# Performance work log

Hardware: AMD Instinct MI355X
Metric: run time of the kernel (lower is better)

## Reference

```python
import jax, jax.numpy as jnp
import numpy as np

BN_EPS = 1e-5


def binary_activation(x):
    # ReActNet binary activation: forward = sign(x), backward = d/dx of
    # piecewise polynomial approximation (straight-through estimator).
    out_fwd = jnp.sign(x)
    out3 = jnp.where(x < -1.0, -1.0,
           jnp.where(x < 0.0, x * x + 2.0 * x,
           jnp.where(x < 1.0, -x * x + 2.0 * x, 1.0)))
    return jax.lax.stop_gradient(out_fwd - out3) + out3


def binarize_weights(w):
    # HardBinaryConv: per-output-channel scale = mean(|w|) (detached),
    # binary weight = scale * sign(w), STE through clamp(w, -1, 1).
    scale = jax.lax.stop_gradient(jnp.mean(jnp.abs(w), axis=(1, 2, 3), keepdims=True))
    bw_no_grad = scale * jnp.sign(w)
    cw = jnp.clip(w, -1.0, 1.0)
    return jax.lax.stop_gradient(bw_no_grad - cw) + cw


def setup_inputs() -> dict:
    key = jax.random.key(0)
    k1, k2, k3, k4 = jax.random.split(key, 4)
    x = jax.random.normal(k1, (32, 256, 56, 56), dtype=jnp.float32)
    weight = jax.random.normal(k2, (256, 256, 3, 3), dtype=jnp.float32) * 0.05  # OIHW
    gamma = 1.0 + 0.1 * jax.random.normal(k3, (256,), dtype=jnp.float32)
    beta = 0.1 * jax.random.normal(k4, (256,), dtype=jnp.float32)
    return {"x": x, "weight": weight, "gamma": gamma, "beta": beta}


def reference(x, weight, gamma, beta):
    xa = binary_activation(x)                       # [B, Cin, H, W], values in {-1, 0, +1}
    bw = binarize_weights(weight)                   # [Cout, Cin, 3, 3]
    y = jax.lax.conv_general_dilated(
        xa, bw,
        window_strides=(1, 1),
        padding=((1, 1), (1, 1)),
        dimension_numbers=("NCHW", "OIHW", "NCHW"))  # [B, Cout, H, W]
    # BatchNorm2d, training-mode batch statistics over (N, H, W)
    mean = jnp.mean(y, axis=(0, 2, 3), keepdims=True)
    var = jnp.var(y, axis=(0, 2, 3), keepdims=True)
    yn = (y - mean) * jax.lax.rsqrt(var + BN_EPS)
    y = yn * gamma[None, :, None, None] + beta[None, :, None, None]
    return jax.nn.relu(y)
```

## Files before the change

### kernel.cpp

```cpp
#include <hip/hip_runtime.h>
#include <stdint.h>
#include <type_traits>

#define CIN   256
#define COUT  256
#define HH    56
#define WW    56
#define HW    3136
#define BATCH 32
#define NPIX  (BATCH*HW)
#define PH    58
#define PW    58
#define PPIX  (PH*PW)
#define KTOT  2304
#define BKB   128
#define NKIT  (KTOT/BKB)

#define NBIN  (HW/64*BATCH)
#define NBRD  (BATCH*PH)

typedef int8_t  i8;
typedef int     intx4  __attribute__((ext_vector_type(4)));
typedef short   short8 __attribute__((ext_vector_type(8)));
typedef float   floatx4 __attribute__((ext_vector_type(4)));

__device__ __forceinline__ void gload_lds16(const i8* g, void* lds_base) {
    __builtin_amdgcn_global_load_lds(
        (const __attribute__((address_space(1))) void*)g,
        (__attribute__((address_space(3))) void*)lds_base,
        16, 0, 0);
}

__global__ __launch_bounds__(256) void front(const float* __restrict__ x,
                                             const float* __restrict__ w,
                                             i8* __restrict__ xs,
                                             i8* __restrict__ wg,
                                             float* __restrict__ scale,
                                             float* __restrict__ bnsum,
                                             float* __restrict__ bnsumsq) {
    int b = blockIdx.x;
    int t = threadIdx.x;
    if (b < NBIN) {
        __shared__ int lds[64 * 65];
        int p0 = (b % 49) * 64;
        int n  = b / 49;
        const float* xin = x + (size_t)n * CIN * HW;
        int pq  = t & 15;
        int cqg = t >> 4;
#pragma unroll
        for (int q = 0; q < 4; ++q) {
            int cbase = q * 64 + cqg * 4;
            floatx4 f[4];
#pragma unroll
            for (int r = 0; r < 4; ++r)
                f[r] = __builtin_nontemporal_load(
                    (const floatx4*)&xin[(size_t)(cbase + r) * HW + p0 + pq * 4]);
#pragma unroll
            for (int j = 0; j < 4; ++j) {
                int packed = 0;
#pragma unroll
                for (int r = 0; r < 4; ++r) {
                    float v = f[r][j];
                    int s = (v > 0.f) ? 1 : ((v < 0.f) ? -1 : 0);
                    packed |= (s & 0xff) << (8 * r);
                }
                lds[(pq * 4 + j) * 65 + q * 16 + cqg] = packed;
            }
        }
        __syncthreads();
        int ci = t & 15;
#pragma unroll
        for (int q = 0; q < 4; ++q) {
            int pi = (t >> 4) + q * 16;
            int4 v;
            v.x = lds[pi * 65 + ci * 4 + 0];
            v.y = lds[pi * 65 + ci * 4 + 1];
            v.z = lds[pi * 65 + ci * 4 + 2];
            v.w = lds[pi * 65 + ci * 4 + 3];
            int p = p0 + pi;
            int h = p / WW, ww = p - (p / WW) * WW;
            *(int4*)&xs[((size_t)n * PPIX + (size_t)(h + 1) * PW + (ww + 1)) * CIN
                        + ci * 16] = v;
        }
    } else if (b < NBIN + COUT) {
        int o = b - NBIN;
        const float* wrow = w + (size_t)o * KTOT + (size_t)t * 9;
        float asum = 0.f;
#pragma unroll
        for (int tt = 0; tt < 9; ++tt) {
            float v = wrow[tt];
            asum += fabsf(v);
            wg[(size_t)o * KTOT + tt * CIN + t] = (v > 0.f) ? (i8)1 : ((v < 0.f) ? (i8)(-1) : (i8)0);
        }
        for (int off = 32; off > 0; off >>= 1) asum += __shfl_down(asum, off);
        __shared__ float red[4];
        if ((t & 63) == 0) red[t >> 6] = asum;
        __syncthreads();
        if (t == 0) {
            scale[o]   = (red[0] + red[1] + red[2] + red[3]) * (1.f / (float)KTOT);
            bnsum[o]   = 0.f;
            bnsumsq[o] = 0.f;
        }
    } else {
        int bb = b - NBIN - COUT;
        int n  = bb / PH;
        int pr = bb % PH;
        int* row = (int*)(xs + ((size_t)n * PPIX + (size_t)pr * PW) * CIN);
        if (pr == 0 || pr == PH - 1) {
            for (int idx = t; idx < PW * CIN / 4; idx += 256) row[idx] = 0;
        } else {
            if (t < 64)       row[t] = 0;
            else if (t < 128) row[(PW - 1) * (CIN / 4) + t - 64] = 0;
        }
    }
}

__global__ __launch_bounds__(256, 2) void conv_gemm(const i8* __restrict__ xs,
                                                    const i8* __restrict__ wg,
                                                    short* __restrict__ y,
                                                    float* __restrict__ bnsum,
                                                    float* __restrict__ bnsumsq) {
    __shared__ __align__(16) i8 smem[65536];

    int tid  = threadIdx.x;
    int lane = tid & 63;
    int wv   = tid >> 6;
    int wm   = wv & 1;
    int wn   = wv >> 1;
    int hb   = blockIdx.x;
    int mt   = ((hb >> 4) << 3) + (hb & 7);
    int nt   = (hb >> 3) & 1;

    int prow = tid >> 3;
    int koff = ((tid ^ (tid >> 3)) & 7) * 16;
    const i8* aP[4];
    const i8* bP[4];
#pragma unroll
    for (int j = 0; j < 4; ++j) {
        int P = mt * 128 + prow + 32 * j;
        int n = P / HW;
        int p = P - n * HW;
        int h = p / WW;
        int w = p - h * WW;
        aP[j] = xs + ((size_t)n * PPIX + (size_t)h * PW + w) * CIN + koff;
        int o = nt * 128 + prow + 32 * j;
        bP[j] = wg + (size_t)o * KTOT + koff;
    }
    i8* aD[2][4];
    i8* bD[2][4];
#pragma unroll
    for (int b = 0; b < 2; ++b)
#pragma unroll
        for (int j = 0; j < 4; ++j) {
            aD[b][j] = smem + b * 32768 + j * 4096 + wv * 1024;
            bD[b][j] = smem + b * 32768 + 16384 + j * 4096 + wv * 1024;
        }

    int l7  = lane & 7;
    int l15 = lane & 15;
    int lhi = lane >> 4;
    int sw0 = ((lhi ^ l7) << 4);
    int sw1 = sw0 ^ 0x40;
    const i8* Ard0 = smem + (wm * 64 + l15) * BKB + sw0;
    const i8* Ard1 = smem + (wm * 64 + l15) * BKB + sw1;
    const i8* Brd0 = smem + 16384 + (wn * 64 + l15) * BKB + sw0;
    const i8* Brd1 = smem + 16384 + (wn * 64 + l15) * BKB + sw1;

    intx4 acc[4][4];
#pragma unroll
    for (int im = 0; im < 4; ++im)
#pragma unroll
        for (int in = 0; in < 4; ++in) acc[im][in] = intx4{0, 0, 0, 0};

#pragma unroll
    for (int j = 0; j < 4; ++j) gload_lds16(aP[j], aD[0][j]);
#pragma unroll
    for (int j = 0; j < 4; ++j) gload_lds16(bP[j], bD[0][j]);
    __syncthreads();

    auto stage = [&](auto KBC) {
        constexpr int KB  = (int)decltype(KBC)::value;
        constexpr int cur = KB & 1;
        if constexpr (KB < NKIT - 1) {
            constexpr int nb  = KB + 1;
            constexpr int nxt = nb & 1;
            constexpr int ao  = (nb / 6) * PW * CIN + (nb % 6) * 128;
            constexpr int bo  = nb * BKB;
#pragma unroll
            for (int j = 0; j < 4; ++j) gload_lds16(aP[j] + ao, aD[nxt][j]);
#pragma unroll
            for (int j = 0; j < 4; ++j) gload_lds16(bP[j] + bo, bD[nxt][j]);
        }
        constexpr int bufo = cur * 32768;
        intx4 af0[4], bf0[4], af1[4], bf1[4];
#pragma unroll
        for (int im = 0; im < 4; ++im) af0[im] = *(const intx4*)(Ard0 + bufo + im * 2048);
#pragma unroll
        for (int in = 0; in < 4; ++in) bf0[in] = *(const intx4*)(Brd0 + bufo + in * 2048);
#pragma unroll
        for (int im = 0; im < 4; ++im) af1[im] = *(const intx4*)(Ard1 + bufo + im * 2048);
#pragma unroll
        for (int in = 0; in < 4; ++in) bf1[in] = *(const intx4*)(Brd1 + bufo + in * 2048);
#pragma unroll
        for (int im = 0; im < 4; ++im)
#pragma unroll
            for (int in = 0; in < 4; ++in)
                acc[im][in] = __builtin_amdgcn_mfma_i32_16x16x64_i8(
                    af0[im], bf0[in], acc[im][in], 0, 0, 0);
#pragma unroll
        for (int im = 0; im < 4; ++im)
#pragma unroll
            for (int in = 0; in < 4; ++in)
                acc[im][in] = __builtin_amdgcn_mfma_i32_16x16x64_i8(
                    af1[im], bf1[in], acc[im][in], 0, 0, 0);
        __syncthreads();
    };
#define ST(k) stage(std::integral_constant<int, k>{});
    ST(0) ST(1) ST(2) ST(3) ST(4) ST(5) ST(6) ST(7) ST(8)
    ST(9) ST(10) ST(11) ST(12) ST(13) ST(14) ST(15) ST(16) ST(17)
#undef ST

    int colBase = nt * 128 + wn * 64 + l15;
    short* yt = (short*)smem;
#pragma unroll
    for (int in = 0; in < 4; ++in) {
        int o = colBase + in * 16;
        float s1 = 0.f, s2 = 0.f;
#pragma unroll
        for (int im = 0; im < 4; ++im) {
            int r0 = wm * 64 + im * 16 + lhi * 4;
#pragma unroll
            for (int rg = 0; rg < 4; ++rg) {
                int vi = acc[im][in][rg];
                yt[(r0 + rg) * 128 + wn * 64 + in * 16 + l15] = (short)vi;
                float v = (float)vi;
                s1 += v;
                s2 += v * v;
            }
        }
        s1 += __shfl_xor(s1, 16); s2 += __shfl_xor(s2, 16);
        s1 += __shfl_xor(s1, 32); s2 += __shfl_xor(s2, 32);
        if (lhi == 0) {
            atomicAdd(&bnsum[o], s1);
            atomicAdd(&bnsumsq[o], s2);
        }
    }
    __syncthreads();
#pragma unroll
    for (int pass = 0; pass < 8; ++pass) {
        int p = (tid >> 4) + 16 * pass;
        int c = tid & 15;
        __builtin_nontemporal_store(
            *(const short8*)&yt[p * 128 + c * 8],
            (short8*)&y[(size_t)(mt * 128 + p) * COUT + nt * 128 + c * 8]);
    }
}

__global__ __launch_bounds__(256) void bn_out(const short* __restrict__ y,
                                              const float* __restrict__ bnsum,
                                              const float* __restrict__ bnsumsq,
                                              const float* __restrict__ scale,
                                              const float* __restrict__ gamma,
                                              const float* __restrict__ beta,
                                              float* __restrict__ out) {
    __shared__ float lds[64 * 65];
    __shared__ float gs[256], cs[256];
    int p0 = blockIdx.x * 64;
    int n  = blockIdx.y;
    int t  = threadIdx.x;

    int cch = t & 7;
    int piA = t >> 3;
    const short* yb = y + ((size_t)n * HW + p0) * COUT;
    short8 sv[4][2];
#pragma unroll
    for (int g = 0; g < 4; ++g)
#pragma unroll
        for (int j = 0; j < 2; ++j)
            sv[g][j] = __builtin_nontemporal_load(
                (const short8*)&yb[(size_t)(piA + 32 * j) * COUT + g * 64 + cch * 8]);

    {
        float mean = bnsum[t] * (1.f / (float)NPIX);
        float var  = fmaxf(bnsumsq[t] * (1.f / (float)NPIX) - mean * mean, 0.f);
        float sc   = scale[t];
        float inv  = rsqrtf(sc * sc * var + 1e-5f);
        float g    = gamma[t] * sc * inv;
        gs[t] = g;
        cs[t] = beta[t] - mean * g;
    }
    __syncthreads();

#pragma unroll
    for (int g = 0; g < 4; ++g) {
        int o0 = g * 64;
#pragma unroll
        for (int j = 0; j < 2; ++j) {
            int pi = piA + 32 * j;
#pragma unroll
            for (int e = 0; e < 8; ++e) {
                int ch = o0 + cch * 8 + e;
                lds[pi * 65 + cch * 8 + e] =
                    fmaxf(gs[ch] * (float)sv[g][j][e] + cs[ch], 0.f);
            }
        }
        __syncthreads();
        float* ob = out + ((size_t)n * COUT + o0) * HW + p0;
        int pq = t & 15;
        int ch = t >> 4;
#pragma unroll
        for (int r = 0; r < 4; ++r) {
            int cr = ch + 16 * r;
            floatx4 v;
#pragma unroll
            for (int e = 0; e < 4; ++e) v[e] = lds[(pq * 4 + e) * 65 + cr];
            __builtin_nontemporal_store(v, (floatx4*)&ob[(size_t)cr * HW + pq * 4]);
        }
        if (g < 3) __syncthreads();
    }
}

extern "C" void kernel_launch(void* const* d_in, const int* in_sizes, int n_in,
                              void* d_out, int out_size, void* d_ws, size_t ws_size,
                              hipStream_t stream) {
    const float* x     = (const float*)d_in[0];
    const float* w     = (const float*)d_in[1];
    const float* gamma = (const float*)d_in[2];
    const float* beta  = (const float*)d_in[3];
    float* out = (float*)d_out;

    char* ws = (char*)d_ws;
    size_t off = 0;
    i8* xs = (i8*)(ws + off);    off += (size_t)BATCH * PPIX * CIN;
    i8* wg = (i8*)(ws + off);    off += (size_t)COUT * KTOT;
    short* y = (short*)(ws + off); off += (size_t)NPIX * COUT * sizeof(short);
    float* scale   = (float*)(ws + off); off += 1024;
    float* bnsum   = (float*)(ws + off); off += 1024;
    float* bnsumsq = (float*)(ws + off); off += 1024;

    hipLaunchKernelGGL(front, dim3(NBIN + COUT + NBRD), dim3(256), 0, stream,
                       x, w, xs, wg, scale, bnsum, bnsumsq);
    hipLaunchKernelGGL(conv_gemm, dim3(NPIX / 128 * 2), dim3(256), 0, stream,
                       xs, wg, y, bnsum, bnsumsq);
    hipLaunchKernelGGL(bn_out, dim3(HW / 64, BATCH), dim3(256), 0, stream,
                       y, bnsum, bnsumsq, scale, gamma, beta, out);
}
```

Baseline: 267.6 us.

## Store conv output channel-major so BN epilogue needs no transpose

The GEMM epilogue now transposes its tile through an XOR-swizzled LDS buffer and writes the int16 intermediate in channel-major [C][N*HW] layout instead of pixel-major. The BN/ReLU kernel then becomes a simple per-(channel, batch) streaming pass with contiguous reads and writes, with no LDS transpose and no barriers. The transpose cost moves into the GEMM epilogue. The BN kernel now has 3136/4 = 784 vector elements per block of 256 threads, so its last loop iteration is only partly filled.

```diff
diff --git a/kernel.cpp b/kernel.cpp
--- a/kernel.cpp
+++ b/kernel.cpp
@@ -21,6 +21,7 @@
 
 typedef int8_t  i8;
 typedef int     intx4  __attribute__((ext_vector_type(4)));
+typedef short   short4v __attribute__((ext_vector_type(4)));
 typedef short   short8 __attribute__((ext_vector_type(8)));
 typedef float   floatx4 __attribute__((ext_vector_type(4)));
 
@@ -220,23 +221,26 @@
     ST(9) ST(10) ST(11) ST(12) ST(13) ST(14) ST(15) ST(16) ST(17)
 #undef ST
 
+    i8* ytb = smem;
     int colBase = nt * 128 + wn * 64 + l15;
-    short* yt = (short*)smem;
 #pragma unroll
     for (int in = 0; in < 4; ++in) {
-        int o = colBase + in * 16;
+        int cl = wn * 64 + in * 16 + l15;
+        int o  = colBase + in * 16;
         float s1 = 0.f, s2 = 0.f;
 #pragma unroll
         for (int im = 0; im < 4; ++im) {
-            int r0 = wm * 64 + im * 16 + lhi * 4;
+            short4v pk;
 #pragma unroll
             for (int rg = 0; rg < 4; ++rg) {
                 int vi = acc[im][in][rg];
-                yt[(r0 + rg) * 128 + wn * 64 + in * 16 + l15] = (short)vi;
+                pk[rg] = (short)vi;
                 float v = (float)vi;
                 s1 += v;
                 s2 += v * v;
             }
+            int p3 = 8 * wm + 2 * im + (lhi >> 1);
+            *(short4v*)(ytb + cl * 256 + ((p3 ^ (cl & 15)) * 16) + (lhi & 1) * 8) = pk;
         }
         s1 += __shfl_xor(s1, 16); s2 += __shfl_xor(s2, 16);
         s1 += __shfl_xor(s1, 32); s2 += __shfl_xor(s2, 32);
@@ -248,11 +252,11 @@
     __syncthreads();
 #pragma unroll
     for (int pass = 0; pass < 8; ++pass) {
-        int p = (tid >> 4) + 16 * pass;
-        int c = tid & 15;
-        __builtin_nontemporal_store(
-            *(const short8*)&yt[p * 128 + c * 8],
-            (short8*)&y[(size_t)(mt * 128 + p) * COUT + nt * 128 + c * 8]);
+        int chl = (tid >> 4) + 16 * pass;
+        int l   = tid & 15;
+        short8 v = *(const short8*)(ytb + chl * 256 + ((l ^ (chl & 15)) * 16));
+        __builtin_nontemporal_store(v,
+            (short8*)&y[(size_t)(nt * 128 + chl) * NPIX + (size_t)mt * 128 + 8 * l]);
     }
 }
 
@@ -263,60 +267,25 @@
                                               const float* __restrict__ gamma,
                                               const float* __restrict__ beta,
                                               float* __restrict__ out) {
-    __shared__ float lds[64 * 65];
-    __shared__ float gs[256], cs[256];
-    int p0 = blockIdx.x * 64;
-    int n  = blockIdx.y;
-    int t  = threadIdx.x;
-
-    int cch = t & 7;
-    int piA = t >> 3;
-    const short* yb = y + ((size_t)n * HW + p0) * COUT;
-    short8 sv[4][2];
-#pragma unroll
-    for (int g = 0; g < 4; ++g)
-#pragma unroll
-        for (int j = 0; j < 2; ++j)
-            sv[g][j] = __builtin_nontemporal_load(
-                (const short8*)&yb[(size_t)(piA + 32 * j) * COUT + g * 64 + cch * 8]);
-
-    {
-        float mean = bnsum[t] * (1.f / (float)NPIX);
-        float var  = fmaxf(bnsumsq[t] * (1.f / (float)NPIX) - mean * mean, 0.f);
-        float sc   = scale[t];
-        float inv  = rsqrtf(sc * sc * var + 1e-5f);
-        float g    = gamma[t] * sc * inv;
-        gs[t] = g;
-        cs[t] = beta[t] - mean * g;
-    }
-    __syncthreads();
-
-#pragma unroll
-    for (int g = 0; g < 4; ++g) {
-        int o0 = g * 64;
-#pragma unroll
-        for (int j = 0; j < 2; ++j) {
-            int pi = piA + 32 * j;
-#pragma unroll
-            for (int e = 0; e < 8; ++e) {
-                int ch = o0 + cch * 8 + e;
-                lds[pi * 65 + cch * 8 + e] =
-                    fmaxf(gs[ch] * (float)sv[g][j][e] + cs[ch], 0.f);
-            }
-        }
-        __syncthreads();
-        float* ob = out + ((size_t)n * COUT + o0) * HW + p0;
-        int pq = t & 15;
-        int ch = t >> 4;
-#pragma unroll
-        for (int r = 0; r < 4; ++r) {
-            int cr = ch + 16 * r;
-            floatx4 v;
-#pragma unroll
-            for (int e = 0; e < 4; ++e) v[e] = lds[(pq * 4 + e) * 65 + cr];
-            __builtin_nontemporal_store(v, (floatx4*)&ob[(size_t)cr * HW + pq * 4]);
-        }
-        if (g < 3) __syncthreads();
+    int c = blockIdx.x;
+    int n = blockIdx.y;
+    int t = threadIdx.x;
+
+    float mean = bnsum[c] * (1.f / (float)NPIX);
+    float var  = fmaxf(bnsumsq[c] * (1.f / (float)NPIX) - mean * mean, 0.f);
+    float sc   = scale[c];
+    float inv  = rsqrtf(sc * sc * var + 1e-5f);
+    float g    = gamma[c] * sc * inv;
+    float cc   = beta[c] - mean * g;
+
+    const short4v* yb = (const short4v*)(y + (size_t)c * NPIX + (size_t)n * HW);
+    floatx4* ob = (floatx4*)(out + ((size_t)n * COUT + c) * HW);
+    for (int i = t; i < HW / 4; i += 256) {
+        short4v s = __builtin_nontemporal_load(&yb[i]);
+        floatx4 v;
+#pragma unroll
+        for (int e = 0; e < 4; ++e) v[e] = fmaxf(g * (float)s[e] + cc, 0.f);
+        __builtin_nontemporal_store(v, &ob[i]);
     }
 }
 
@@ -342,6 +311,6 @@
                        x, w, xs, wg, scale, bnsum, bnsumsq);
     hipLaunchKernelGGL(conv_gemm, dim3(NPIX / 128 * 2), dim3(256), 0, stream,
                        xs, wg, y, bnsum, bnsumsq);
-    hipLaunchKernelGGL(bn_out, dim3(HW / 64, BATCH), dim3(256), 0, stream,
+    hipLaunchKernelGGL(bn_out, dim3(COUT, BATCH), dim3(256), 0, stream,
                        y, bnsum, bnsumsq, scale, gamma, beta, out);
 }
```

Result: no change. 265.9 us (median of 2 runs) (-0.7%).
